# Optimization experiments

Measured on AMD Instinct MI355X. Metric: run time of the kernel, lower is better.

The kernel has to match this reference:

```python
import jax, jax.numpy as jnp
import numpy as np

EPS = 1e-5
HEADS, DQK, DV, SD = 1, 12, 12, 2  # heads, dim_qk, dim_v, spatial_down


def group_norm(x, w, b):
    # GroupNorm(1, C): normalize over all non-batch dims, per-channel affine
    axes = tuple(range(1, x.ndim))
    m = x.mean(axis=axes, keepdims=True)
    v = x.var(axis=axes, keepdims=True)
    xn = (x - m) * jax.lax.rsqrt(v + EPS)
    shp = (1, -1) + (1,) * (x.ndim - 2)
    return xn * w.reshape(shp) + b.reshape(shp)


def setup_inputs() -> dict:
    key = jax.random.key(0)
    ks = jax.random.split(key, 6)
    B, Ccv, D, H, W = 4, 32, 48, 64, 128
    Cf, Hs, Ws = 256, 8, 16  # Hs*Ws = 128 == max_tokens -> token_pool is identity
    cost = jax.random.normal(ks[0], (B, Ccv, D, H, W), jnp.float32)
    feat_s4 = jax.random.normal(ks[1], (B, Cf, Hs, Ws), jnp.float32)
    E = HEADS * DQK
    w_q = jax.random.normal(ks[2], (E, Ccv), jnp.float32) * (1.0 / np.sqrt(Ccv))
    w_k = jax.random.normal(ks[3], (E, Cf), jnp.float32) * (1.0 / np.sqrt(Cf))
    w_v = jax.random.normal(ks[4], (HEADS * DV, Cf), jnp.float32) * (1.0 / np.sqrt(Cf))
    w_out = jax.random.normal(ks[5], (Ccv, HEADS * DV), jnp.float32) * (1.0 / np.sqrt(HEADS * DV))
    return {
        'cost': cost, 'feat_s4': feat_s4,
        'w_q': w_q, 'w_k': w_k, 'w_v': w_v, 'w_out': w_out,
        'gn_in_w': jnp.ones((Ccv,), jnp.float32), 'gn_in_b': jnp.zeros((Ccv,), jnp.float32),
        'gn_out_w': jnp.ones((Ccv,), jnp.float32), 'gn_out_b': jnp.zeros((Ccv,), jnp.float32),
        'gamma': jnp.float32(0.1),
    }


def reference(cost, feat_s4, w_q, w_k, w_v, w_out, gn_in_w, gn_in_b, gn_out_w, gn_out_b, gamma):
    B, Ccv, D, H, W = cost.shape
    x_in = group_norm(cost, gn_in_w, gn_in_b)
    # avg_pool3d kernel/stride (1, SD, SD)
    Hq, Wq = H // SD, W // SD
    xq = x_in.reshape(B, Ccv, D, Hq, SD, Wq, SD).mean(axis=(4, 6))
    # 1x1 conv projections == channel matmuls
    q = jnp.einsum('bcdhw,ec->bedhw', xq, w_q)          # (B, h*dqk, D, Hq, Wq)
    k = jnp.einsum('bchw,ec->behw', feat_s4, w_k)       # (B, h*dqk, Hs, Ws)
    v = jnp.einsum('bchw,ec->behw', feat_s4, w_v)       # (B, h*dv, Hs, Ws)
    Ns = k.shape[2] * k.shape[3]
    kf = k.reshape(B, HEADS, DQK, Ns)                   # (B, h, dqk, Ns)
    vf = v.reshape(B, HEADS, DV, Ns)                    # (B, h, dv, Ns)
    N = D * Hq * Wq
    qf = q.reshape(B, HEADS, DQK, N).transpose(0, 1, 3, 2)  # (B, h, N, dqk)
    logits = jnp.einsum('bhnq,bhqs->bhns', qf, kf) * (DQK ** -0.5)
    attn = jax.nn.softmax(logits, axis=-1)
    out = jnp.einsum('bhns,bhds->bhnd', attn, vf)       # (B, h, N, dv)
    out = out.transpose(0, 1, 3, 2).reshape(B, HEADS * DV, D, Hq, Wq)
    out = jnp.einsum('bedhw,ce->bcdhw', out, w_out)     # (B, Ccv, D, Hq, Wq)
    # trilinear upsample (align_corners=False == half-pixel, jax.image default)
    out = jax.image.resize(out, (B, Ccv, D, H, W), method='trilinear')
    out = out.astype(jnp.bfloat16).astype(jnp.float32)  # replicate torch bf16 cast
    return group_norm(cost + gamma * out, gn_out_w, gn_out_b)
```

## Files before the change

### kernel.cpp

```cpp
#include <hip/hip_runtime.h>

typedef float f4v __attribute__((ext_vector_type(4)));

namespace {
constexpr int Bn = 4, Cn = 32, Dn = 48, Hn = 64, Wn = 128;
constexpr int HQ = 32, WQ = 64;
constexpr int NPB = Dn * HQ * WQ;
constexpr int DHW = Dn * Hn * Wn;
constexpr int PERB = Cn * DHW;
constexpr int NS = 128, En = 12;
constexpr float EPS = 1e-5f;
constexpr float SQK = 0.2886751345948129f;
constexpr int NB1 = 384;
constexpr int NBA = 128;

constexpr size_t OFF_ZB  = 0;
constexpr size_t OFF_QP  = 6291456;
constexpr size_t OFF_P1  = OFF_QP + 4718592;
constexpr size_t OFF_P2  = OFF_P1 + 3072;
constexpr size_t OFF_PKV = OFF_P2 + 2048;
}

__device__ inline unsigned short bf16b(float x) {
    unsigned u = __float_as_uint(x);
    return (unsigned short)((u + 0x7fffu + ((u >> 16) & 1u)) >> 16);
}
__device__ inline float b2f(unsigned short h) { return __uint_as_float(((unsigned)h) << 16); }
__device__ inline float bf16_rne(float x) {
    unsigned u = __float_as_uint(x);
    u = (u + 0x7fffu + ((u >> 16) & 1u)) & 0xffff0000u;
    return __uint_as_float(u);
}

__device__ inline float2 block_red2(float s, float ss) {
#pragma unroll
    for (int off = 32; off; off >>= 1) {
        s += __shfl_down(s, off, 64);
        ss += __shfl_down(ss, off, 64);
    }
    __shared__ float red[8];
    int lane = threadIdx.x & 63, w = threadIdx.x >> 6;
    __syncthreads();
    if (!lane) { red[w] = s; red[4 + w] = ss; }
    __syncthreads();
    return make_float2(red[0] + red[1] + red[2] + red[3],
                       red[4] + red[5] + red[6] + red[7]);
}

__global__ __launch_bounds__(256) void k1_pool(const float* __restrict__ cost,
                                               const float* __restrict__ feat,
                                               const float* __restrict__ w_q,
                                               const float* __restrict__ w_k,
                                               const float* __restrict__ w_v,
                                               const float* __restrict__ w_out,
                                               const float* __restrict__ gniw,
                                               unsigned* __restrict__ qp,
                                               float2* __restrict__ part1,
                                               float* __restrict__ pkv) {
    __shared__ float wqg[En * Cn], WOs[Cn * En];
    const int b = blockIdx.y, tid = threadIdx.x;
    for (int i = tid; i < En * Cn; i += 256) {
        wqg[i] = w_q[i] * gniw[i & 31];
        WOs[i] = w_out[i];
    }
    __syncthreads();
    const int n = blockIdx.x * 256 + tid;
    const int d = n >> 11, r = n & 2047, hq = r >> 6, wq = r & 63;
    const float* base = cost + (size_t)b * PERB + (size_t)d * 8192 + (hq * 2) * Wn + wq * 2;
    float s = 0.f, ss = 0.f;
    float q[En], pw[En];
#pragma unroll
    for (int e = 0; e < En; ++e) { q[e] = 0.f; pw[e] = 0.f; }
#pragma unroll 4
    for (int c = 0; c < Cn; ++c) {
        const float* src = base + (size_t)c * DHW;
        float2 t0 = *reinterpret_cast<const float2*>(src);
        float2 t1 = *reinterpret_cast<const float2*>(src + Wn);
        float ps = t0.x + t0.y + t1.x + t1.y;
        s += ps;
        ss += t0.x * t0.x + t0.y * t0.y + t1.x * t1.x + t1.y * t1.y;
        float pv = 0.25f * ps;
#pragma unroll
        for (int e = 0; e < En; ++e) {
            q[e] += wqg[e * Cn + c] * pv;
            pw[e] += WOs[c * En + e] * pv;
        }
    }
#pragma unroll
    for (int e = 0; e < En; ++e) {
        unsigned pk = (unsigned)bf16b(q[e]) | ((unsigned)bf16b(pw[e]) << 16);
        __builtin_nontemporal_store(pk, qp + (size_t)(b * En + e) * NPB + n);
    }
    float2 rp = block_red2(s, ss);
    if (!tid) part1[b * NB1 + blockIdx.x] = rp;

    if (b == 0 && blockIdx.x < 16 && tid < NS) {
        const int g = blockIdx.x, kb = g >> 2, cg = g & 3, sI = tid;
        float kk[En], vv[En];
#pragma unroll
        for (int e = 0; e < En; ++e) { kk[e] = 0.f; vv[e] = 0.f; }
        for (int ch = 0; ch < 4; ++ch) {
            const int c0 = cg * 64 + ch * 16;
            float f[16];
#pragma unroll
            for (int jj = 0; jj < 16; ++jj) f[jj] = feat[(size_t)(kb * 256 + c0 + jj) * NS + sI];
#pragma unroll
            for (int jj = 0; jj < 16; ++jj) {
                const int c = c0 + jj;
#pragma unroll
                for (int e = 0; e < En; ++e) {
                    kk[e] += w_k[e * 256 + c] * f[jj];
                    vv[e] += w_v[e * 256 + c] * f[jj];
                }
            }
        }
#pragma unroll
        for (int e = 0; e < En; ++e) {
            pkv[((size_t)(g * NS + sI)) * 24 + e] = kk[e];
            pkv[((size_t)(g * NS + sI)) * 24 + 12 + e] = vv[e];
        }
    }
}

__global__ __launch_bounds__(256) void k_attn(const unsigned* __restrict__ qp,
                                              const float* __restrict__ pkv,
                                              const float* __restrict__ w_q,
                                              const float* __restrict__ gniw,
                                              const float* __restrict__ gnib,
                                              const float2* __restrict__ part1,
                                              const float* __restrict__ w_out,
                                              unsigned short* __restrict__ zb,
                                              float4* __restrict__ part2) {
    __shared__ float Ks[NS * En], Vs[NS * En], WOs[Cn * En], QBs[En];
    __shared__ float G[En * En], woSum[En];
    __shared__ float kred[2], kscs_sh;
    const int x = blockIdx.x, b = blockIdx.y, tid = threadIdx.x;
    const int u = tid >> 6, lane = tid & 63;

    float sP = 0.f, ssP = 0.f;
    for (int i = tid; i < NB1; i += 256) {
        float2 v = part1[b * NB1 + i];
        sP += v.x; ssP += v.y;
    }
    float2 tP = block_red2(sP, ssP);
    const float mGN = tP.x / (float)PERB;
    const float rsGN = rsqrtf(tP.y / (float)PERB - mGN * mGN + EPS);
    const float qsc = rsGN * SQK;

    for (int i = tid; i < NS * En; i += 256) {
        int s = i / En, e = i - s * En;
        size_t base = ((size_t)((b * 4) * NS + s)) * 24 + e;
        Ks[i] = pkv[base] + pkv[base + 3072] + pkv[base + 6144] + pkv[base + 9216];
        Vs[i] = pkv[base + 12] + pkv[base + 3084] + pkv[base + 6156] + pkv[base + 9228];
    }
    for (int i = tid; i < Cn * En; i += 256) WOs[i] = w_out[i];
    if (tid < En) {
        float acc = 0.f;
        for (int c = 0; c < Cn; ++c)
            acc += w_q[tid * Cn + c] * (gnib[c] - mGN * rsGN * gniw[c]);
        QBs[tid] = SQK * acc;
    }
    __syncthreads();
    if (tid < 144) {
        int e1 = tid / 12, e2 = tid - e1 * 12;
        float a = 0.f;
        for (int c = 0; c < Cn; ++c) a += WOs[c * En + e1] * WOs[c * En + e2];
        G[tid] = a;
    }
    if (tid >= 144 && tid < 156) {
        int e = tid - 144;
        float a = 0.f;
        for (int c = 0; c < Cn; ++c) a += WOs[c * En + e];
        woSum[e] = a;
    }
    if (tid < NS) {
        float n2 = 0.f;
#pragma unroll
        for (int e = 0; e < En; ++e) { float k = Ks[tid * En + e]; n2 += k * k; }
#pragma unroll
        for (int off = 32; off; off >>= 1) n2 = fmaxf(n2, __shfl_down(n2, off, 64));
        if (!(tid & 63)) kred[tid >> 6] = n2;
    }
    __syncthreads();
    if (!tid) kscs_sh = sqrtf(fmaxf(kred[0], kred[1]));
    __syncthreads();
    const float kscs = kscs_sh;

    int npos[3];
#pragma unroll
    for (int p = 0; p < 3; ++p) npos[p] = x * 768 + (u * 3 + p) * 64 + lane;

    f4v q[3][3];
    float ub[3];
#pragma unroll
    for (int p = 0; p < 3; ++p) {
        const int n = npos[p];
        float qn2 = 0.f;
#pragma unroll
        for (int v = 0; v < 3; ++v) {
            f4v t;
#pragma unroll
            for (int uu = 0; uu < 4; ++uu) {
                int e = v * 4 + uu;
                unsigned pk = __builtin_nontemporal_load(qp + (size_t)(b * En + e) * NPB + n);
                float qe = qsc * b2f((unsigned short)(pk & 0xffffu)) + QBs[e];
                t[uu] = qe;
                qn2 += qe * qe;
            }
            q[p][v] = t;
        }
        ub[p] = sqrtf(qn2) * kscs;
    }

    f4v o0[3], o1[3], o2[3];
    float l[3];
#pragma unroll
    for (int p = 0; p < 3; ++p) {
        o0[p] = (f4v)(0.f); o1[p] = (f4v)(0.f); o2[p] = (f4v)(0.f);
        l[p] = 0.f;
    }
    const f4v* K4 = (const f4v*)Ks;
    const f4v* V4 = (const f4v*)Vs;
    for (int s = 0; s < NS; ++s) {
        f4v k0 = K4[s * 3], k1 = K4[s * 3 + 1], k2 = K4[s * 3 + 2];
        f4v v0 = V4[s * 3], v1 = V4[s * 3 + 1], v2 = V4[s * 3 + 2];
#pragma unroll
        for (int p = 0; p < 3; ++p) {
            f4v d4 = q[p][0] * k0 + q[p][1] * k1 + q[p][2] * k2;
            float dot = (d4.x + d4.y) + (d4.z + d4.w);
            float pe = __expf(dot - ub[p]);
            l[p] += pe;
            o0[p] += pe * v0; o1[p] += pe * v1; o2[p] += pe * v2;
        }
    }

    float hv[3][En];
#pragma unroll
    for (int p = 0; p < 3; ++p) {
        float iv = 1.0f / l[p];
#pragma unroll
        for (int uu = 0; uu < 4; ++uu) {
            hv[p][uu] = o0[p][uu] * iv;
            hv[p][4 + uu] = o1[p][uu] * iv;
            hv[p][8 + uu] = o2[p][uu] * iv;
        }
    }

    for (int c = 0; c < Cn; ++c) {
        float z[3];
#pragma unroll
        for (int p = 0; p < 3; ++p) {
            float a = 0.f;
#pragma unroll
            for (int e = 0; e < En; ++e) a += WOs[c * En + e] * hv[p][e];
            z[p] = a;
        }
#pragma unroll
        for (int p = 0; p < 3; ++p)
            __builtin_nontemporal_store(bf16b(z[p]),
                                        zb + (size_t)(b * Cn + c) * NPB + npos[p]);
    }

    float sz = 0.f, spz = 0.f;
#pragma unroll
    for (int p = 0; p < 3; ++p) {
#pragma unroll
        for (int e = 0; e < En; ++e) {
            sz += woSum[e] * hv[p][e];
            unsigned pk = __builtin_nontemporal_load(qp + (size_t)(b * En + e) * NPB + npos[p]);
            spz += b2f((unsigned short)(pk >> 16)) * hv[p][e];
        }
    }

    const bool okw = (lane < 63);
    float hs[3][En];
#pragma unroll
    for (int p = 0; p < 3; ++p)
#pragma unroll
        for (int e = 0; e < En; ++e) {
            float t = __shfl_down(hv[p][e], 1, 64);
            hs[p][e] = okw ? t : 0.f;
        }

    float hD[3];
    bool hOk[3];
#pragma unroll
    for (int p = 0; p < 3; ++p) {
        int h = (x * 12 + u * 3 + p) & 31;
        hD[p] = (h == 0 || h == 31) ? 1.625f : 1.25f;
        hOk[p] = (h < 31) && (p < 2);
    }
    const float Dw = (lane == 0 || lane == 63) ? 1.625f : 1.25f;

    float t2 = 0.f;
#pragma unroll
    for (int p = 0; p < 3; ++p) {
        float Gh[En];
#pragma unroll
        for (int e = 0; e < En; ++e) {
            float a = 0.f;
#pragma unroll
            for (int f = 0; f < En; ++f) a += G[e * En + f] * hv[p][f];
            Gh[e] = a;
        }
        float gpp = 0.f, gw = 0.f;
#pragma unroll
        for (int e = 0; e < En; ++e) {
            gpp += Gh[e] * hv[p][e];
            gw += Gh[e] * hs[p][e];
        }
        t2 += hD[p] * Dw * gpp + 0.75f * hD[p] * gw;
        if (p < 2 && hOk[p]) {
            float ghp = 0.f, gd1 = 0.f;
#pragma unroll
            for (int e = 0; e < En; ++e) {
                ghp += Gh[e] * hv[p + 1][e];
                gd1 += Gh[e] * hs[p + 1][e];
            }
            t2 += 0.75f * Dw * ghp + 0.28125f * gd1;
        }
        if (p > 0 && hOk[p - 1]) {
            float gd2 = 0.f;
#pragma unroll
            for (int e = 0; e < En; ++e) gd2 += Gh[e] * hs[p - 1][e];
            t2 += 0.28125f * gd2;
        }
    }
    float2 rA = block_red2(sz, spz);
    float2 rB = block_red2(t2, 0.f);
    if (!tid) part2[b * NBA + x] = make_float4(rA.x, rA.y, rB.x, 0.f);
}

__global__ __launch_bounds__(256) void k_final(const float* __restrict__ cost,
                                               const unsigned short* __restrict__ zb,
                                               const float* __restrict__ gamma_p,
                                               const float2* __restrict__ part1,
                                               const float4* __restrict__ part2,
                                               const float* __restrict__ gow,
                                               const float* __restrict__ gob,
                                               float* __restrict__ out) {
    const int blk = blockIdx.x;
    const int b = blk / (Cn * Dn);
    const int c = (blk / Dn) % Cn;
    const int tid = threadIdx.x;
    const float g = gamma_p[0];

    float sc_ = 0.f, scc = 0.f;
    for (int i = tid; i < NB1; i += 256) {
        float2 v = part1[b * NB1 + i];
        sc_ += v.x; scc += v.y;
    }
    float2 tA = block_red2(sc_, scc);
    float sz = 0.f, spz = 0.f, t2 = 0.f;
    if (tid < NBA) {
        float4 v = part2[b * NBA + tid];
        sz = v.x; spz = v.y; t2 = v.z;
    }
    float2 tB = block_red2(sz, spz);
    float2 tC = block_red2(t2, 0.f);
    const float Sy = tA.x + 4.f * g * tB.x;
    const float Syy = tA.y + 8.f * g * tB.y + g * g * tC.x;
    const float m = Sy / (float)PERB;
    const float var = Syy / (float)PERB - m * m;
    const float rs = rsqrtf(var + EPS);

    __shared__ float zs[HQ * WQ];
    {
        const unsigned int* zsrc = (const unsigned int*)(zb + (size_t)blk * 2048);
        for (int i = tid; i < 1024; i += 256) {
            unsigned v = __builtin_nontemporal_load(zsrc + i);
            zs[2 * i] = b2f((unsigned short)(v & 0xffffu));
            zs[2 * i + 1] = b2f((unsigned short)(v >> 16));
        }
    }
    __syncthreads();
    const float sc = rs * gow[c], bi = gob[c];
    const f4v* cq = (const f4v*)(cost + (size_t)blk * 8192);
    f4v* oq = (f4v*)(out + (size_t)blk * 8192);

    const int hbase = tid >> 5;
    const int w4 = (tid & 31) << 2;
    const float wh0 = (hbase & 1) ? 0.75f : 0.25f;
    const float wh1 = 1.0f - wh0;
    const int ia = (w4 >> 1) - 1 < 0 ? 0 : (w4 >> 1) - 1;
    const int ib = w4 >> 1;
    const int ic = (w4 >> 1) + 1;
    const int id = (w4 >> 1) + 2 > WQ - 1 ? WQ - 1 : (w4 >> 1) + 2;

#pragma unroll
    for (int k = 0; k < 8; ++k) {
        const int h = hbase + 8 * k;
        int h0 = (h - 1) >> 1;
        h0 = h0 < 0 ? 0 : h0;
        int h1 = h0 + 1;
        h1 = h1 > HQ - 1 ? HQ - 1 : h1;
        const float* r0 = zs + h0 * WQ;
        const float* r1 = zs + h1 * WQ;
        const float a0 = r0[ia], b0 = r0[ib], c0 = r0[ic], d0 = r0[id];
        const float a1 = r1[ia], b1 = r1[ib], c1 = r1[ic], d1 = r1[id];
        const float t0j = 0.25f * a0 + 0.75f * b0, u0j = 0.25f * a1 + 0.75f * b1;
        const float t1j = 0.75f * b0 + 0.25f * c0, u1j = 0.75f * b1 + 0.25f * c1;
        const float t2j = 0.25f * b0 + 0.75f * c0, u2j = 0.25f * b1 + 0.75f * c1;
        const float t3j = 0.75f * c0 + 0.25f * d0, u3j = 0.75f * c1 + 0.25f * d1;
        const int qd = tid + 256 * k;
        f4v cv = cq[qd];
        f4v ov;
        ov.x = (cv.x + g * bf16_rne(wh0 * t0j + wh1 * u0j) - m) * sc + bi;
        ov.y = (cv.y + g * bf16_rne(wh0 * t1j + wh1 * u1j) - m) * sc + bi;
        ov.z = (cv.z + g * bf16_rne(wh0 * t2j + wh1 * u2j) - m) * sc + bi;
        ov.w = (cv.w + g * bf16_rne(wh0 * t3j + wh1 * u3j) - m) * sc + bi;
        __builtin_nontemporal_store(ov, oq + qd);
    }
}

extern "C" void kernel_launch(void* const* d_in, const int* in_sizes, int n_in,
                              void* d_out, int out_size, void* d_ws, size_t ws_size,
                              hipStream_t stream) {
    const float* cost  = (const float*)d_in[0];
    const float* feat  = (const float*)d_in[1];
    const float* w_q   = (const float*)d_in[2];
    const float* w_k   = (const float*)d_in[3];
    const float* w_v   = (const float*)d_in[4];
    const float* w_out = (const float*)d_in[5];
    const float* gniw  = (const float*)d_in[6];
    const float* gnib  = (const float*)d_in[7];
    const float* gow   = (const float*)d_in[8];
    const float* gob   = (const float*)d_in[9];
    const float* gamma = (const float*)d_in[10];

    float* ws = (float*)d_ws;
    float* outp = (float*)d_out;

    unsigned short* zb = (unsigned short*)(ws + OFF_ZB);
    unsigned* qp = (unsigned*)(ws + OFF_QP);
    float2* part1 = (float2*)(ws + OFF_P1);
    float4* part2 = (float4*)(ws + OFF_P2);
    float* pkv = ws + OFF_PKV;

    k1_pool<<<dim3(NB1, Bn), 256, 0, stream>>>(cost, feat, w_q, w_k, w_v, w_out, gniw,
                                               qp, part1, pkv);
    k_attn<<<dim3(NBA, Bn), 256, 0, stream>>>(qp, pkv, w_q, gniw, gnib, part1,
                                              w_out, zb, part2);
    k_final<<<Bn * Cn * Dn, 256, 0, stream>>>(cost, zb, gamma, part1, part2, gow, gob, outp);
}
```

Before: 173.7 us.

## Hoist final GroupNorm stats into tiny kernel and reuse packed q loads

The output GroupNorm statistics were recomputed by each of the 6144 blocks of k_final. They are now reduced once per batch in a new four-block kernel that writes mean and rstd, and k_final reads two floats. k_attn now keeps the high halves of the packed qp words from its first load, so it no longer reloads qp for the spz term. qp stores and loads also switch from nontemporal to ordinary accesses. The extra kernel launch adds a small serial step between k_attn and k_final.

```diff
diff --git a/kernel.cpp b/kernel.cpp
--- a/kernel.cpp
+++ b/kernel.cpp
@@ -18,7 +18,8 @@
 constexpr size_t OFF_QP  = 6291456;
 constexpr size_t OFF_P1  = OFF_QP + 4718592;
 constexpr size_t OFF_P2  = OFF_P1 + 3072;
-constexpr size_t OFF_PKV = OFF_P2 + 2048;
+constexpr size_t OFF_ST2 = OFF_P2 + 2048;
+constexpr size_t OFF_PKV = OFF_ST2 + 8;
 }
 
 __device__ inline unsigned short bf16b(float x) {
@@ -89,7 +90,7 @@
 #pragma unroll
     for (int e = 0; e < En; ++e) {
         unsigned pk = (unsigned)bf16b(q[e]) | ((unsigned)bf16b(pw[e]) << 16);
-        __builtin_nontemporal_store(pk, qp + (size_t)(b * En + e) * NPB + n);
+        qp[(size_t)(b * En + e) * NPB + n] = pk;
     }
     float2 rp = block_red2(s, ss);
     if (!tid) part1[b * NB1 + blockIdx.x] = rp;
@@ -190,6 +191,7 @@
 #pragma unroll
     for (int p = 0; p < 3; ++p) npos[p] = x * 768 + (u * 3 + p) * 64 + lane;
 
+    float pwv[3][En];
     f4v q[3][3];
     float ub[3];
 #pragma unroll
@@ -202,8 +204,9 @@
 #pragma unroll
             for (int uu = 0; uu < 4; ++uu) {
                 int e = v * 4 + uu;
-                unsigned pk = __builtin_nontemporal_load(qp + (size_t)(b * En + e) * NPB + n);
+                unsigned pk = qp[(size_t)(b * En + e) * NPB + n];
                 float qe = qsc * b2f((unsigned short)(pk & 0xffffu)) + QBs[e];
+                pwv[p][e] = b2f((unsigned short)(pk >> 16));
                 t[uu] = qe;
                 qn2 += qe * qe;
             }
@@ -267,8 +270,7 @@
 #pragma unroll
         for (int e = 0; e < En; ++e) {
             sz += woSum[e] * hv[p][e];
-            unsigned pk = __builtin_nontemporal_load(qp + (size_t)(b * En + e) * NPB + npos[p]);
-            spz += b2f((unsigned short)(pk >> 16)) * hv[p][e];
+            spz += pwv[p][e] * hv[p][e];
         }
     }
 
@@ -331,11 +333,38 @@
     if (!tid) part2[b * NBA + x] = make_float4(rA.x, rA.y, rB.x, 0.f);
 }
 
+__global__ __launch_bounds__(256) void k_st2(const float2* __restrict__ part1,
+                                             const float4* __restrict__ part2,
+                                             const float* __restrict__ gamma_p,
+                                             float2* __restrict__ st2) {
+    const int b = blockIdx.x, tid = threadIdx.x;
+    const float g = gamma_p[0];
+    float sc_ = 0.f, scc = 0.f;
+    for (int i = tid; i < NB1; i += 256) {
+        float2 v = part1[b * NB1 + i];
+        sc_ += v.x; scc += v.y;
+    }
+    float2 tA = block_red2(sc_, scc);
+    float sz = 0.f, spz = 0.f, t2 = 0.f;
+    if (tid < NBA) {
+        float4 v = part2[b * NBA + tid];
+        sz = v.x; spz = v.y; t2 = v.z;
+    }
+    float2 tB = block_red2(sz, spz);
+    float2 tC = block_red2(t2, 0.f);
+    if (!tid) {
+        const float Sy = tA.x + 4.f * g * tB.x;
+        const float Syy = tA.y + 8.f * g * tB.y + g * g * tC.x;
+        const float m = Sy / (float)PERB;
+        const float var = Syy / (float)PERB - m * m;
+        st2[b] = make_float2(m, rsqrtf(var + EPS));
+    }
+}
+
 __global__ __launch_bounds__(256) void k_final(const float* __restrict__ cost,
                                                const unsigned short* __restrict__ zb,
                                                const float* __restrict__ gamma_p,
-                                               const float2* __restrict__ part1,
-                                               const float4* __restrict__ part2,
+                                               const float2* __restrict__ st2,
                                                const float* __restrict__ gow,
                                                const float* __restrict__ gob,
                                                float* __restrict__ out) {
@@ -344,25 +373,8 @@
     const int c = (blk / Dn) % Cn;
     const int tid = threadIdx.x;
     const float g = gamma_p[0];
-
-    float sc_ = 0.f, scc = 0.f;
-    for (int i = tid; i < NB1; i += 256) {
-        float2 v = part1[b * NB1 + i];
-        sc_ += v.x; scc += v.y;
-    }
-    float2 tA = block_red2(sc_, scc);
-    float sz = 0.f, spz = 0.f, t2 = 0.f;
-    if (tid < NBA) {
-        float4 v = part2[b * NBA + tid];
-        sz = v.x; spz = v.y; t2 = v.z;
-    }
-    float2 tB = block_red2(sz, spz);
-    float2 tC = block_red2(t2, 0.f);
-    const float Sy = tA.x + 4.f * g * tB.x;
-    const float Syy = tA.y + 8.f * g * tB.y + g * g * tC.x;
-    const float m = Sy / (float)PERB;
-    const float var = Syy / (float)PERB - m * m;
-    const float rs = rsqrtf(var + EPS);
+    const float2 st = st2[b];
+    const float m = st.x, rs = st.y;
 
     __shared__ float zs[HQ * WQ];
     {
@@ -435,11 +447,13 @@
     unsigned* qp = (unsigned*)(ws + OFF_QP);
     float2* part1 = (float2*)(ws + OFF_P1);
     float4* part2 = (float4*)(ws + OFF_P2);
+    float2* st2 = (float2*)(ws + OFF_ST2);
     float* pkv = ws + OFF_PKV;
 
     k1_pool<<<dim3(NB1, Bn), 256, 0, stream>>>(cost, feat, w_q, w_k, w_v, w_out, gniw,
                                                qp, part1, pkv);
     k_attn<<<dim3(NBA, Bn), 256, 0, stream>>>(qp, pkv, w_q, gniw, gnib, part1,
                                               w_out, zb, part2);
-    k_final<<<Bn * Cn * Dn, 256, 0, stream>>>(cost, zb, gamma, part1, part2, gow, gob, outp);
-}
+    k_st2<<<Bn, 256, 0, stream>>>(part1, part2, gamma, st2);
+    k_final<<<Bn * Cn * Dn, 256, 0, stream>>>(cost, zb, gamma, st2, gow, gob, outp);
+}
```

New measurement: 172.9 us. Within noise of the previous version (-0.5%).
